# Kernel tuning notes

Hardware: AMD Instinct MI355X
Metric: run time of the kernel (lower is better)

The kernel has to match this reference:

```python
import jax, jax.numpy as jnp
import numpy as np
from jax import lax

EMBED_DIM = 384
NUM_GROUPS = 128
GROUP_SIZE = 64
LN_EPS = 1e-5


def setup_inputs() -> dict:
    key = jax.random.key(0)
    k_pts, k1, k2, k3, k4 = jax.random.split(key, 5)
    B, N = 32, 16384
    points = jax.random.normal(k_pts, (B, N, 3), dtype=jnp.float32)
    # local_mlp: Linear(3,128) -> GELU -> Linear(128, embed_dim)
    w1 = jax.random.normal(k1, (3, 128), dtype=jnp.float32) * (1.0 / np.sqrt(3))
    b1 = jax.random.normal(k2, (128,), dtype=jnp.float32) * 0.01
    w2 = jax.random.normal(k3, (128, EMBED_DIM), dtype=jnp.float32) * (1.0 / np.sqrt(128))
    b2 = jax.random.normal(k4, (EMBED_DIM,), dtype=jnp.float32) * 0.01
    ln_scale = jnp.ones((EMBED_DIM,), dtype=jnp.float32)
    ln_bias = jnp.zeros((EMBED_DIM,), dtype=jnp.float32)
    return {"points": points, "w1": w1, "b1": b1, "w2": w2, "b2": b2,
            "ln_scale": ln_scale, "ln_bias": ln_bias}


def _farthest_point_sample(points, num_samples):
    # points: [B, N, 3]. Deterministic start at index 0 (torch uses randint).
    B, N, _ = points.shape

    def step(carry, _):
        distance, farthest = carry  # [B, N], [B]
        centroid = jnp.take_along_axis(points, farthest[:, None, None], axis=1)  # [B,1,3]
        d = jnp.sum((points - centroid) ** 2, axis=-1)  # [B, N]
        distance = jnp.minimum(distance, d)
        nxt = jnp.argmax(distance, axis=-1).astype(jnp.int32)
        return (distance, nxt), farthest

    init = (jnp.full((B, N), jnp.inf, dtype=points.dtype),
            jnp.zeros((B,), dtype=jnp.int32))
    _, idx = lax.scan(step, init, None, length=num_samples)  # [S, B]
    return idx.T  # [B, S]


def reference(points, w1, b1, w2, b2, ln_scale, ln_bias):
    B, N, _ = points.shape
    centroid_idx = _farthest_point_sample(points, NUM_GROUPS)  # [B, G]
    centroids = jnp.take_along_axis(
        points, centroid_idx[:, :, None].astype(jnp.int32), axis=1)  # [B, G, 3]

    # squared distances (same ordering as torch.cdist for topk); matmul form
    # avoids materializing a [B, G, N, 3] diff tensor.
    c2 = jnp.sum(centroids ** 2, axis=-1)  # [B, G]
    p2 = jnp.sum(points ** 2, axis=-1)     # [B, N]
    dist2 = c2[:, :, None] + p2[:, None, :] - 2.0 * jnp.einsum(
        'bgc,bnc->bgn', centroids, points)  # [B, G, N]

    # k smallest -> top_k of negated distances
    _, neighbor_idx = lax.top_k(-dist2, GROUP_SIZE)  # [B, G, K]

    batch_ix = jnp.arange(B)[:, None, None]
    grouped = points[batch_ix, neighbor_idx]  # [B, G, K, 3]
    local_coords = grouped - centroids[:, :, None, :]  # [B, G, K, 3]

    h = jax.nn.gelu(local_coords @ w1 + b1, approximate=False)  # [B,G,K,128]
    feats = h @ w2 + b2  # [B, G, K, D]
    tokens = jnp.mean(feats, axis=2)  # [B, G, D]

    mu = jnp.mean(tokens, axis=-1, keepdims=True)
    var = jnp.mean((tokens - mu) ** 2, axis=-1, keepdims=True)
    tokens_ln = (tokens - mu) * lax.rsqrt(var + LN_EPS) * ln_scale + ln_bias
    return centroids, tokens_ln
```

## Files before the change

### kernel.cpp

```cpp
#include <hip/hip_runtime.h>
#include <math.h>

#define BB 32
#define NN 16384
#define GG 128
#define KK 64
#define HH 128
#define DD 384
#define LN_EPS 1e-5f
#define NBUCK 2048
#define CANDCAP 1024

__device__ __forceinline__ float sq3(float x, float y, float z) {
    return __fadd_rn(__fadd_rn(__fmul_rn(x, x), __fmul_rn(y, y)), __fmul_rn(z, z));
}

__device__ __forceinline__ unsigned distkey(float px, float py, float pz, float4 c4) {
    float p2 = sq3(px, py, pz);
    float dot = __fadd_rn(__fadd_rn(__fmul_rn(c4.x, px), __fmul_rn(c4.y, py)),
                          __fmul_rn(c4.z, pz));
    float d = __fsub_rn(__fadd_rn(c4.w, p2), __fmul_rn(2.0f, dot));
    unsigned u = __float_as_uint(d);
    return u ^ ((u & 0x80000000u) ? 0xFFFFFFFFu : 0x80000000u);
}

__global__ void prep_kernel(const float* __restrict__ w2, float* __restrict__ w2t) {
    int i = blockIdx.x * 256 + threadIdx.x;
    if (i < HH * DD) {
        int f = i >> 7;
        int k = i & 127;
        w2t[i] = w2[k * DD + f];
    }
}

__global__ __launch_bounds__(512, 2) void fps_kernel(const float* __restrict__ pts,
                                                     float* __restrict__ cent_out,
                                                     float4* __restrict__ cent_pad) {
    const int b = blockIdx.x;
    const int tid = threadIdx.x;
    const float* p = pts + (size_t)b * NN * 3;
    const float4* p4 = (const float4*)p;

    float x[32], y[32], z[32], dist[32];
#pragma unroll
    for (int j = 0; j < 8; j++) {
        int q = j * 512 + tid;
        float4 A = p4[3 * q], B = p4[3 * q + 1], C = p4[3 * q + 2];
        x[j * 4 + 0] = A.x; y[j * 4 + 0] = A.y; z[j * 4 + 0] = A.z;
        x[j * 4 + 1] = A.w; y[j * 4 + 1] = B.x; z[j * 4 + 1] = B.y;
        x[j * 4 + 2] = B.z; y[j * 4 + 2] = B.w; z[j * 4 + 2] = C.x;
        x[j * 4 + 3] = C.y; y[j * 4 + 3] = C.z; z[j * 4 + 3] = C.w;
#pragma unroll
        for (int t = 0; t < 4; t++) dist[j * 4 + t] = INFINITY;
    }

    __shared__ unsigned long long slot[GG];
    for (int i = tid; i < GG; i += 512) slot[i] = 0ull;
    __syncthreads();

    float cx = p[0], cy = p[1], cz = p[2];

    for (int it = 0; it < GG; it++) {
        if (tid == 0) {
            float* co = cent_out + ((size_t)b * GG + it) * 3;
            co[0] = cx; co[1] = cy; co[2] = cz;
            cent_pad[b * GG + it] = make_float4(cx, cy, cz, sq3(cx, cy, cz));
        }
        if (it == GG - 1) break;

        float bv0 = -INFINITY, bv1 = -INFINITY, bv2 = -INFINITY, bv3 = -INFINITY;
        int bi0 = 0, bi1 = 0, bi2 = 0, bi3 = 0;
#pragma unroll
        for (int j = 0; j < 8; j++) {
            int nb = 4 * (j * 512 + tid);
#pragma unroll
            for (int t = 0; t < 4; t++) {
                int r = j * 4 + t;
                float dx = __fsub_rn(x[r], cx);
                float dy = __fsub_rn(y[r], cy);
                float dz = __fsub_rn(z[r], cz);
                float d = sq3(dx, dy, dz);
                float dj = fminf(dist[r], d);
                dist[r] = dj;
                int n = nb + t;
                switch (t) {
                    case 0: if (dj > bv0) { bv0 = dj; bi0 = n; } break;
                    case 1: if (dj > bv1) { bv1 = dj; bi1 = n; } break;
                    case 2: if (dj > bv2) { bv2 = dj; bi2 = n; } break;
                    case 3: if (dj > bv3) { bv3 = dj; bi3 = n; } break;
                }
            }
        }
        float fv = bv0; int fi = bi0;
        if (bv1 > fv || (bv1 == fv && bi1 < fi)) { fv = bv1; fi = bi1; }
        if (bv2 > fv || (bv2 == fv && bi2 < fi)) { fv = bv2; fi = bi2; }
        if (bv3 > fv || (bv3 == fv && bi3 < fi)) { fv = bv3; fi = bi3; }
#pragma unroll
        for (int off = 32; off >= 1; off >>= 1) {
            float ov = __shfl_down(fv, off);
            int oi = __shfl_down(fi, off);
            if (ov > fv || (ov == fv && oi < fi)) { fv = ov; fi = oi; }
        }
        if ((tid & 63) == 0) {
            unsigned long long packed =
                ((unsigned long long)__float_as_uint(fv) << 32) |
                (unsigned)(0xFFFFFFFFu - (unsigned)fi);
            atomicMax(&slot[it], packed);
        }
        __syncthreads();
        unsigned long long w = slot[it];
        int idx = (int)(0xFFFFFFFFu - (unsigned)w);
        const float* wp = p + (size_t)idx * 3;
        cx = wp[0]; cy = wp[1]; cz = wp[2];
    }
}

__global__ __launch_bounds__(256, 6) void group_kernel(
    const float* __restrict__ pts, const float4* __restrict__ cent_pad,
    const float* __restrict__ w1, const float* __restrict__ b1,
    const float* __restrict__ w2t, const float* __restrict__ b2,
    const float* __restrict__ lns, const float* __restrict__ lnb,
    float* __restrict__ tok_out) {
    __shared__ __align__(16) union {
        unsigned hist[NBUCK];
        unsigned long long cand[CANDCAP];
    } sh;
    __shared__ int selIdx[KK];
    __shared__ float4 localPt[KK];
    __shared__ float w1s[3 * HH];
    __shared__ float b1s[HH];
    __shared__ __align__(16) float hbar[HH];
    __shared__ float partial[256];
    __shared__ float red2[8];
    __shared__ float toks[DD];
    __shared__ int waveSum[4];
    __shared__ unsigned long long wmin[4];
    __shared__ unsigned TA_S;
    __shared__ int cntS;
    __shared__ unsigned long long lastS;
    __shared__ float muS, rstdS;

    const int tid = threadIdx.x;
    int bid = blockIdx.x;
    int xcd = bid & 7, sub = bid >> 3;
    int b = xcd * 4 + (sub >> 7);
    int g = sub & 127;

    const float* p = pts + (size_t)b * NN * 3;
    const float4* p4 = (const float4*)p;
    float4 c4 = cent_pad[b * GG + g];

    for (int i = tid; i < 3 * HH; i += 256) w1s[i] = w1[i];
    if (tid < HH) b1s[tid] = b1[tid];
    for (int i = tid; i < NBUCK; i += 256) sh.hist[i] = 0;
    if (tid == 0) cntS = 0;
    __syncthreads();

    for (int i = 0; i < 16; i++) {
        int t4 = i * 256 + tid;
        float4 A = p4[3 * t4], B = p4[3 * t4 + 1], C = p4[3 * t4 + 2];
        unsigned k0 = distkey(A.x, A.y, A.z, c4);
        unsigned k1 = distkey(A.w, B.x, B.y, c4);
        unsigned k2 = distkey(B.z, B.w, C.x, c4);
        unsigned k3 = distkey(C.y, C.z, C.w, c4);
        atomicAdd(&sh.hist[k0 >> 21], 1u);
        atomicAdd(&sh.hist[k1 >> 21], 1u);
        atomicAdd(&sh.hist[k2 >> 21], 1u);
        atomicAdd(&sh.hist[k3 >> 21], 1u);
    }
    __syncthreads();

    {
        uint4 h0 = ((const uint4*)sh.hist)[tid * 2];
        uint4 h1 = ((const uint4*)sh.hist)[tid * 2 + 1];
        int loc[8] = {(int)h0.x, (int)h0.y, (int)h0.z, (int)h0.w,
                      (int)h1.x, (int)h1.y, (int)h1.z, (int)h1.w};
        int s = 0;
#pragma unroll
        for (int j = 0; j < 8; j++) s += loc[j];
        int lane = tid & 63, wid = tid >> 6;
        int v = s;
#pragma unroll
        for (int off = 1; off < 64; off <<= 1) {
            int o = __shfl_up(v, off);
            if (lane >= off) v += o;
        }
        if (lane == 63) waveSum[wid] = v;
        __syncthreads();
        int base = 0;
        for (int w = 0; w < wid; w++) base += waveSum[w];
        int c = base + v - s;
#pragma unroll
        for (int j = 0; j < 8; j++) {
            if (c < KK && c + loc[j] >= KK) TA_S = (unsigned)(tid * 8 + j);
            c += loc[j];
        }
        __syncthreads();
    }
    unsigned TA = TA_S;

    for (int i = 0; i < 16; i++) {
        int t4 = i * 256 + tid;
        float4 A = p4[3 * t4], B = p4[3 * t4 + 1], C = p4[3 * t4 + 2];
        unsigned k[4];
        k[0] = distkey(A.x, A.y, A.z, c4);
        k[1] = distkey(A.w, B.x, B.y, c4);
        k[2] = distkey(B.z, B.w, C.x, c4);
        k[3] = distkey(C.y, C.z, C.w, c4);
#pragma unroll
        for (int q = 0; q < 4; q++) {
            if ((k[q] >> 21) <= TA) {
                int pos = atomicAdd(&cntS, 1);
                if (pos < CANDCAP)
                    sh.cand[pos] =
                        ((unsigned long long)k[q] << 32) | (unsigned)(4 * t4 + q);
            }
        }
    }
    __syncthreads();
    int cnt = cntS;

    if (cnt <= CANDCAP) {
        for (int c0 = tid; c0 < cnt; c0 += 256) {
            unsigned long long pr = sh.cand[c0];
            int rank = 0;
            for (int j = 0; j < cnt; j++) rank += (sh.cand[j] < pr);
            if (rank < KK) selIdx[rank] = (int)(unsigned)pr;
        }
        __syncthreads();
    } else {
        if (tid == 0) lastS = 0ull;
        __syncthreads();
        for (int r = 0; r < KK; r++) {
            unsigned long long last = lastS;
            unsigned long long best = 0xFFFFFFFFFFFFFFFFull;
            for (int i = 0; i < 16; i++) {
                int t4 = i * 256 + tid;
                float4 A = p4[3 * t4], B = p4[3 * t4 + 1], C = p4[3 * t4 + 2];
                unsigned k[4];
                k[0] = distkey(A.x, A.y, A.z, c4);
                k[1] = distkey(A.w, B.x, B.y, c4);
                k[2] = distkey(B.z, B.w, C.x, c4);
                k[3] = distkey(C.y, C.z, C.w, c4);
#pragma unroll
                for (int q = 0; q < 4; q++) {
                    unsigned long long pr =
                        ((unsigned long long)k[q] << 32) | (unsigned)(4 * t4 + q);
                    if ((r == 0 || pr > last) && pr < best) best = pr;
                }
            }
            unsigned blo = (unsigned)best, bhi = (unsigned)(best >> 32);
#pragma unroll
            for (int off = 32; off >= 1; off >>= 1) {
                unsigned olo = __shfl_down(blo, off);
                unsigned ohi = __shfl_down(bhi, off);
                unsigned long long ob = ((unsigned long long)ohi << 32) | olo;
                unsigned long long cur = ((unsigned long long)bhi << 32) | blo;
                if (ob < cur) { blo = olo; bhi = ohi; }
            }
            int lane = tid & 63, wid = tid >> 6;
            if (lane == 0) wmin[wid] = ((unsigned long long)bhi << 32) | blo;
            __syncthreads();
            if (tid == 0) {
                unsigned long long m = wmin[0];
                for (int w = 1; w < 4; w++) if (wmin[w] < m) m = wmin[w];
                selIdx[r] = (int)(unsigned)m;
                lastS = m;
            }
            __syncthreads();
        }
    }

    if (tid < KK) {
        int n = selIdx[tid];
        float px = p[n * 3], py = p[n * 3 + 1], pz = p[n * 3 + 2];
        localPt[tid] = make_float4(px - c4.x, py - c4.y, pz - c4.z, 0.f);
    }
    __syncthreads();
    {
        int f = tid & 127, half = tid >> 7;
        float wa = w1s[f], wb = w1s[HH + f], wc = w1s[2 * HH + f], bb = b1s[f];
        float s = 0.f;
        for (int k = half * 32; k < half * 32 + 32; k++) {
            float4 lp = localPt[k];
            float a = lp.x * wa + lp.y * wb + lp.z * wc + bb;
            float hh = 0.5f * a * (1.0f + erff(a * 0.70710678118654752440f));
            s += hh;
        }
        partial[tid] = s;
    }
    __syncthreads();
    if (tid < HH) hbar[tid] = (partial[tid] + partial[tid + HH]) * (1.0f / 64.0f);
    __syncthreads();
    for (int f2 = tid; f2 < DD; f2 += 256) {
        const float4* wrow = (const float4*)(w2t + f2 * HH);
        const float4* hb = (const float4*)hbar;
        float acc = b2[f2];
#pragma unroll 8
        for (int q = 0; q < 32; q++) {
            float4 w4 = wrow[q];
            float4 h4 = hb[q];
            acc += h4.x * w4.x + h4.y * w4.y + h4.z * w4.z + h4.w * w4.w;
        }
        toks[f2] = acc;
    }
    __syncthreads();
    {
        float s1 = 0.f, s2 = 0.f;
        for (int f2 = tid; f2 < DD; f2 += 256) {
            float v = toks[f2];
            s1 += v;
            s2 += v * v;
        }
#pragma unroll
        for (int off = 32; off >= 1; off >>= 1) {
            s1 += __shfl_down(s1, off);
            s2 += __shfl_down(s2, off);
        }
        int lane = tid & 63, wid = tid >> 6;
        if (lane == 0) { partial[wid] = s1; red2[wid] = s2; }
        __syncthreads();
        if (tid == 0) {
            float t1 = partial[0] + partial[1] + partial[2] + partial[3];
            float t2 = red2[0] + red2[1] + red2[2] + red2[3];
            float mu = t1 / (float)DD;
            float var = t2 / (float)DD - mu * mu;
            muS = mu;
            rstdS = rsqrtf(var + LN_EPS);
        }
        __syncthreads();
    }
    float mu = muS, rstd = rstdS;
    float* outp = tok_out + ((size_t)b * GG + g) * DD;
    for (int f2 = tid; f2 < DD; f2 += 256) {
        outp[f2] = (toks[f2] - mu) * rstd * lns[f2] + lnb[f2];
    }
}

extern "C" void kernel_launch(void* const* d_in, const int* in_sizes, int n_in,
                              void* d_out, int out_size, void* d_ws, size_t ws_size,
                              hipStream_t stream) {
    const float* pts = (const float*)d_in[0];
    const float* w1 = (const float*)d_in[1];
    const float* b1 = (const float*)d_in[2];
    const float* w2 = (const float*)d_in[3];
    const float* b2 = (const float*)d_in[4];
    const float* lns = (const float*)d_in[5];
    const float* lnb = (const float*)d_in[6];
    float* out = (float*)d_out;

    float4* cent_pad = (float4*)d_ws;
    float* w2t = (float*)((char*)d_ws + BB * GG * sizeof(float4));

    prep_kernel<<<192, 256, 0, stream>>>(w2, w2t);
    fps_kernel<<<BB, 512, 0, stream>>>(pts, out, cent_pad);
    group_kernel<<<BB * GG, 256, 0, stream>>>(pts, cent_pad, w1, b1, w2t, b2, lns, lnb,
                                              out + BB * GG * 3);
}
```

Measured before the change: 531.7 us.

## Split farthest-point sampling across eight blocks per batch with global-memory barrier

Farthest-point sampling now runs on 8 cooperating blocks per batch of 256 threads each, instead of one 512-thread block, so 256 blocks occupy many more CUs. Each block finds its local farthest point, writes a packed key and the point's coordinates to global memory, and spins on an atomic counter until all 8 slices arrive. All blocks then reduce the 8 candidates redundantly. Carrying the coordinates through the reduction removes the dependent global load of the winner's coordinates. The cost is a per-iteration inter-block spin barrier through L2, which relies on all 256 blocks being co-resident to avoid deadlock.

```diff
diff --git a/kernel.cpp b/kernel.cpp
--- a/kernel.cpp
+++ b/kernel.cpp
@@ -10,6 +10,7 @@
 #define LN_EPS 1e-5f
 #define NBUCK 2048
 #define CANDCAP 1024
+#define SPB 8
 
 __device__ __forceinline__ float sq3(float x, float y, float z) {
     return __fadd_rn(__fadd_rn(__fmul_rn(x, x), __fmul_rn(y, y)), __fmul_rn(z, z));
@@ -24,27 +25,32 @@
     return u ^ ((u & 0x80000000u) ? 0xFFFFFFFFu : 0x80000000u);
 }
 
-__global__ void prep_kernel(const float* __restrict__ w2, float* __restrict__ w2t) {
+__global__ void prep_kernel(const float* __restrict__ w2, float* __restrict__ w2t,
+                            unsigned* __restrict__ cnt) {
     int i = blockIdx.x * 256 + threadIdx.x;
     if (i < HH * DD) {
         int f = i >> 7;
         int k = i & 127;
         w2t[i] = w2[k * DD + f];
     }
-}
-
-__global__ __launch_bounds__(512, 2) void fps_kernel(const float* __restrict__ pts,
-                                                     float* __restrict__ cent_out,
-                                                     float4* __restrict__ cent_pad) {
-    const int b = blockIdx.x;
+    if (i < BB * GG) cnt[i] = 0;
+}
+
+__global__ __launch_bounds__(256) void fps_kernel(
+    const float* __restrict__ pts, float* __restrict__ cent_out,
+    float4* __restrict__ cent_pad, unsigned long long* __restrict__ candK,
+    float4* __restrict__ candP, unsigned* __restrict__ cnt) {
+    const int blk = blockIdx.x;
+    const int b = blk >> 3;
+    const int s = blk & 7;
     const int tid = threadIdx.x;
     const float* p = pts + (size_t)b * NN * 3;
     const float4* p4 = (const float4*)p;
 
-    float x[32], y[32], z[32], dist[32];
-#pragma unroll
-    for (int j = 0; j < 8; j++) {
-        int q = j * 512 + tid;
+    float x[8], y[8], z[8], dist[8];
+#pragma unroll
+    for (int j = 0; j < 2; j++) {
+        int q = s * 512 + j * 256 + tid;
         float4 A = p4[3 * q], B = p4[3 * q + 1], C = p4[3 * q + 2];
         x[j * 4 + 0] = A.x; y[j * 4 + 0] = A.y; z[j * 4 + 0] = A.z;
         x[j * 4 + 1] = A.w; y[j * 4 + 1] = B.x; z[j * 4 + 1] = B.y;
@@ -54,25 +60,24 @@
         for (int t = 0; t < 4; t++) dist[j * 4 + t] = INFINITY;
     }
 
-    __shared__ unsigned long long slot[GG];
-    for (int i = tid; i < GG; i += 512) slot[i] = 0ull;
-    __syncthreads();
+    __shared__ unsigned long long wkey[4];
+    __shared__ float4 wc[4];
 
     float cx = p[0], cy = p[1], cz = p[2];
 
     for (int it = 0; it < GG; it++) {
-        if (tid == 0) {
+        if (s == 0 && tid == 0) {
             float* co = cent_out + ((size_t)b * GG + it) * 3;
             co[0] = cx; co[1] = cy; co[2] = cz;
             cent_pad[b * GG + it] = make_float4(cx, cy, cz, sq3(cx, cy, cz));
         }
         if (it == GG - 1) break;
 
-        float bv0 = -INFINITY, bv1 = -INFINITY, bv2 = -INFINITY, bv3 = -INFINITY;
-        int bi0 = 0, bi1 = 0, bi2 = 0, bi3 = 0;
-#pragma unroll
-        for (int j = 0; j < 8; j++) {
-            int nb = 4 * (j * 512 + tid);
+        float fv = -INFINITY, fx = 0.f, fy = 0.f, fz = 0.f;
+        int fi = 0;
+#pragma unroll
+        for (int j = 0; j < 2; j++) {
+            int nb = 4 * (s * 512 + j * 256 + tid);
 #pragma unroll
             for (int t = 0; t < 4; t++) {
                 int r = j * 4 + t;
@@ -82,36 +87,58 @@
                 float d = sq3(dx, dy, dz);
                 float dj = fminf(dist[r], d);
                 dist[r] = dj;
-                int n = nb + t;
-                switch (t) {
-                    case 0: if (dj > bv0) { bv0 = dj; bi0 = n; } break;
-                    case 1: if (dj > bv1) { bv1 = dj; bi1 = n; } break;
-                    case 2: if (dj > bv2) { bv2 = dj; bi2 = n; } break;
-                    case 3: if (dj > bv3) { bv3 = dj; bi3 = n; } break;
-                }
-            }
-        }
-        float fv = bv0; int fi = bi0;
-        if (bv1 > fv || (bv1 == fv && bi1 < fi)) { fv = bv1; fi = bi1; }
-        if (bv2 > fv || (bv2 == fv && bi2 < fi)) { fv = bv2; fi = bi2; }
-        if (bv3 > fv || (bv3 == fv && bi3 < fi)) { fv = bv3; fi = bi3; }
+                if (dj > fv) { fv = dj; fi = nb + t; fx = x[r]; fy = y[r]; fz = z[r]; }
+            }
+        }
 #pragma unroll
         for (int off = 32; off >= 1; off >>= 1) {
             float ov = __shfl_down(fv, off);
             int oi = __shfl_down(fi, off);
-            if (ov > fv || (ov == fv && oi < fi)) { fv = ov; fi = oi; }
-        }
-        if ((tid & 63) == 0) {
-            unsigned long long packed =
-                ((unsigned long long)__float_as_uint(fv) << 32) |
-                (unsigned)(0xFFFFFFFFu - (unsigned)fi);
-            atomicMax(&slot[it], packed);
-        }
-        __syncthreads();
-        unsigned long long w = slot[it];
-        int idx = (int)(0xFFFFFFFFu - (unsigned)w);
-        const float* wp = p + (size_t)idx * 3;
-        cx = wp[0]; cy = wp[1]; cz = wp[2];
+            float ox = __shfl_down(fx, off);
+            float oy = __shfl_down(fy, off);
+            float oz = __shfl_down(fz, off);
+            if (ov > fv || (ov == fv && oi < fi)) {
+                fv = ov; fi = oi; fx = ox; fy = oy; fz = oz;
+            }
+        }
+        int lane = tid & 63, wid = tid >> 6;
+        if (lane == 0) {
+            wkey[wid] = ((unsigned long long)__float_as_uint(fv) << 32) |
+                        (unsigned)(0xFFFFFFFFu - (unsigned)fi);
+            wc[wid] = make_float4(fx, fy, fz, 0.f);
+        }
+        __syncthreads();
+
+        const int slot = b * GG + it;
+        if (tid == 0) {
+            unsigned long long bk = wkey[0];
+            float4 bc = wc[0];
+#pragma unroll
+            for (int w = 1; w < 4; w++) {
+                unsigned long long k2 = wkey[w];
+                if (k2 > bk) { bk = k2; bc = wc[w]; }
+            }
+            candK[slot * SPB + s] = bk;
+            candP[slot * SPB + s] = bc;
+            __hip_atomic_fetch_add(&cnt[slot], 1u, __ATOMIC_RELEASE,
+                                   __HIP_MEMORY_SCOPE_AGENT);
+            while (__hip_atomic_load(&cnt[slot], __ATOMIC_ACQUIRE,
+                                     __HIP_MEMORY_SCOPE_AGENT) < SPB)
+                __builtin_amdgcn_s_sleep(1);
+        }
+        __syncthreads();
+
+        {
+            unsigned long long bk = candK[slot * SPB];
+            float4 bc = candP[slot * SPB];
+#pragma unroll
+            for (int w = 1; w < SPB; w++) {
+                unsigned long long k2 = candK[slot * SPB + w];
+                float4 c2 = candP[slot * SPB + w];
+                if (k2 > bk) { bk = k2; bc = c2; }
+            }
+            cx = bc.x; cy = bc.y; cz = bc.z;
+        }
     }
 }
 
@@ -350,10 +377,13 @@
     float* out = (float*)d_out;
 
     float4* cent_pad = (float4*)d_ws;
-    float* w2t = (float*)((char*)d_ws + BB * GG * sizeof(float4));
-
-    prep_kernel<<<192, 256, 0, stream>>>(w2, w2t);
-    fps_kernel<<<BB, 512, 0, stream>>>(pts, out, cent_pad);
+    float* w2t = (float*)((char*)d_ws + 64 * 1024);
+    unsigned long long* candK = (unsigned long long*)((char*)d_ws + 256 * 1024);
+    float4* candP = (float4*)((char*)d_ws + 512 * 1024);
+    unsigned* cnt = (unsigned*)((char*)d_ws + 1024 * 1024);
+
+    prep_kernel<<<192, 256, 0, stream>>>(w2, w2t, cnt);
+    fps_kernel<<<BB * SPB, 256, 0, stream>>>(pts, out, cent_pad, candK, candP, cnt);
     group_kernel<<<BB * GG, 256, 0, stream>>>(pts, cent_pad, w1, b1, w2t, b2, lns, lnb,
                                               out + BB * GG * 3);
 }
```

Measured after the change: 1.134 ms. +113.3%, slower.

## Fuse FPS and grouping into one kernel with progress-flag producer/consumer overlap

Applied to the files above, without the earlier changes.

Merges the farthest-point-sampling and grouping kernels into one launch. The first 32 blocks run FPS at raised priority and publish each centroid plus a per-batch progress counter with agent-scope atomics. The remaining blocks spin-wait on that counter, so kNN grouping for early centroids overlaps the serial FPS iterations instead of waiting for all of FPS to finish. Grouping blocks are widened to 512 threads, with two independent centroid-groups per block using split shared memory. The fused path relies on the FPS blocks being resident (deadlock risk if they are not scheduled) and adds spin-wait and memory-ordering overhead.

```diff
diff --git a/kernel.cpp b/kernel.cpp
--- a/kernel.cpp
+++ b/kernel.cpp
@@ -24,183 +24,237 @@
     return u ^ ((u & 0x80000000u) ? 0xFFFFFFFFu : 0x80000000u);
 }
 
-__global__ void prep_kernel(const float* __restrict__ w2, float* __restrict__ w2t) {
+__global__ void prep_kernel(const float* __restrict__ w2, float* __restrict__ w2t,
+                            unsigned* __restrict__ prog) {
     int i = blockIdx.x * 256 + threadIdx.x;
     if (i < HH * DD) {
         int f = i >> 7;
         int k = i & 127;
         w2t[i] = w2[k * DD + f];
     }
+    if (i < BB) prog[i] = 0;
 }
 
-__global__ __launch_bounds__(512, 2) void fps_kernel(const float* __restrict__ pts,
-                                                     float* __restrict__ cent_out,
-                                                     float4* __restrict__ cent_pad) {
-    const int b = blockIdx.x;
+struct GrpSh {
+    union {
+        unsigned hist[2][NBUCK];
+        unsigned long long cand[2][CANDCAP];
+    } u;
+    int selIdx[2][KK];
+    float4 localPt[2][KK];
+    float w1s[3 * HH];
+    float b1s[HH];
+    float hbar[2][HH];
+    float partial[2][256];
+    float red2[2][4];
+    float toks[2][DD];
+    int waveSum[2][4];
+    unsigned long long wmin[2][4];
+    unsigned TA_S[2];
+    int cntS[2];
+    unsigned long long lastS[2];
+    float muS[2], rstdS[2];
+    float4 c4s[2];
+    int fbS;
+};
+struct FpsSh {
+    unsigned long long slot[GG];
+};
+
+__global__ __launch_bounds__(512, 6) void fused_kernel(
+    const float* __restrict__ pts, const float* __restrict__ w1,
+    const float* __restrict__ b1, const float* __restrict__ w2t,
+    const float* __restrict__ b2, const float* __restrict__ lns,
+    const float* __restrict__ lnb, float* __restrict__ cent_out,
+    float4* __restrict__ cent_pad, float* __restrict__ tok_out,
+    unsigned* __restrict__ prog) {
+    __shared__ union {
+        FpsSh f;
+        GrpSh g;
+    } sh;
     const int tid = threadIdx.x;
+
+    if (blockIdx.x < BB) {
+        __builtin_amdgcn_s_setprio(3);
+        const int b = blockIdx.x;
+        const float* p = pts + (size_t)b * NN * 3;
+        const float4* p4 = (const float4*)p;
+
+        float x[32], y[32], z[32], dist[32];
+#pragma unroll
+        for (int j = 0; j < 8; j++) {
+            int q = j * 512 + tid;
+            float4 A = p4[3 * q], B = p4[3 * q + 1], C = p4[3 * q + 2];
+            x[j * 4 + 0] = A.x; y[j * 4 + 0] = A.y; z[j * 4 + 0] = A.z;
+            x[j * 4 + 1] = A.w; y[j * 4 + 1] = B.x; z[j * 4 + 1] = B.y;
+            x[j * 4 + 2] = B.z; y[j * 4 + 2] = B.w; z[j * 4 + 2] = C.x;
+            x[j * 4 + 3] = C.y; y[j * 4 + 3] = C.z; z[j * 4 + 3] = C.w;
+#pragma unroll
+            for (int t = 0; t < 4; t++) dist[j * 4 + t] = INFINITY;
+        }
+
+        for (int i = tid; i < GG; i += 512) sh.f.slot[i] = 0ull;
+        __syncthreads();
+
+        float cx = p[0], cy = p[1], cz = p[2];
+
+        for (int it = 0; it < GG; it++) {
+            if (tid == 0) {
+                if (it > 0) {
+                    asm volatile("s_waitcnt vmcnt(0)" ::: "memory");
+                    __hip_atomic_store(&prog[b], (unsigned)it, __ATOMIC_RELAXED,
+                                       __HIP_MEMORY_SCOPE_AGENT);
+                }
+                float* co = cent_out + ((size_t)b * GG + it) * 3;
+                co[0] = cx; co[1] = cy; co[2] = cz;
+                float c2v = sq3(cx, cy, cz);
+                unsigned long long lo =
+                    ((unsigned long long)__float_as_uint(cy) << 32) | __float_as_uint(cx);
+                unsigned long long hi =
+                    ((unsigned long long)__float_as_uint(c2v) << 32) | __float_as_uint(cz);
+                unsigned long long* cp =
+                    (unsigned long long*)&cent_pad[(size_t)b * GG + it];
+                __hip_atomic_store(cp, lo, __ATOMIC_RELAXED, __HIP_MEMORY_SCOPE_AGENT);
+                __hip_atomic_store(cp + 1, hi, __ATOMIC_RELAXED, __HIP_MEMORY_SCOPE_AGENT);
+            }
+            if (it == GG - 1) break;
+
+            float bv0 = -INFINITY, bv1 = -INFINITY, bv2 = -INFINITY, bv3 = -INFINITY;
+            int bi0 = 0, bi1 = 0, bi2 = 0, bi3 = 0;
+#pragma unroll
+            for (int j = 0; j < 8; j++) {
+                int nb = 4 * (j * 512 + tid);
+#pragma unroll
+                for (int t = 0; t < 4; t++) {
+                    int r = j * 4 + t;
+                    float dx = __fsub_rn(x[r], cx);
+                    float dy = __fsub_rn(y[r], cy);
+                    float dz = __fsub_rn(z[r], cz);
+                    float d = sq3(dx, dy, dz);
+                    float dj = fminf(dist[r], d);
+                    dist[r] = dj;
+                    int n = nb + t;
+                    switch (t) {
+                        case 0: if (dj > bv0) { bv0 = dj; bi0 = n; } break;
+                        case 1: if (dj > bv1) { bv1 = dj; bi1 = n; } break;
+                        case 2: if (dj > bv2) { bv2 = dj; bi2 = n; } break;
+                        case 3: if (dj > bv3) { bv3 = dj; bi3 = n; } break;
+                    }
+                }
+            }
+            float fv = bv0; int fi = bi0;
+            if (bv1 > fv || (bv1 == fv && bi1 < fi)) { fv = bv1; fi = bi1; }
+            if (bv2 > fv || (bv2 == fv && bi2 < fi)) { fv = bv2; fi = bi2; }
+            if (bv3 > fv || (bv3 == fv && bi3 < fi)) { fv = bv3; fi = bi3; }
+#pragma unroll
+            for (int off = 32; off >= 1; off >>= 1) {
+                float ov = __shfl_down(fv, off);
+                int oi = __shfl_down(fi, off);
+                if (ov > fv || (ov == fv && oi < fi)) { fv = ov; fi = oi; }
+            }
+            if ((tid & 63) == 0) {
+                unsigned long long packed =
+                    ((unsigned long long)__float_as_uint(fv) << 32) |
+                    (unsigned)(0xFFFFFFFFu - (unsigned)fi);
+                atomicMax(&sh.f.slot[it], packed);
+            }
+            __syncthreads();
+            unsigned long long w = sh.f.slot[it];
+            int idx = (int)(0xFFFFFFFFu - (unsigned)w);
+            const float* wp = p + (size_t)idx * 3;
+            cx = wp[0]; cy = wp[1]; cz = wp[2];
+        }
+        if (tid == 0) {
+            asm volatile("s_waitcnt vmcnt(0)" ::: "memory");
+            __hip_atomic_store(&prog[b], (unsigned)GG, __ATOMIC_RELAXED,
+                               __HIP_MEMORY_SCOPE_AGENT);
+        }
+        return;
+    }
+
+    const int h = tid & 255;
+    const int half = tid >> 8;
+    const int lane = h & 63, wid = h >> 6;
+
+    int bid = blockIdx.x - BB;
+    int x = bid & 7;
+    int r = bid >> 3;
+    int g = r >> 1;
+    int pairSel = r & 1;
+    int b = x * 4 + pairSel * 2 + half;
+
     const float* p = pts + (size_t)b * NN * 3;
     const float4* p4 = (const float4*)p;
 
-    float x[32], y[32], z[32], dist[32];
-#pragma unroll
-    for (int j = 0; j < 8; j++) {
-        int q = j * 512 + tid;
-        float4 A = p4[3 * q], B = p4[3 * q + 1], C = p4[3 * q + 2];
-        x[j * 4 + 0] = A.x; y[j * 4 + 0] = A.y; z[j * 4 + 0] = A.z;
-        x[j * 4 + 1] = A.w; y[j * 4 + 1] = B.x; z[j * 4 + 1] = B.y;
-        x[j * 4 + 2] = B.z; y[j * 4 + 2] = B.w; z[j * 4 + 2] = C.x;
-        x[j * 4 + 3] = C.y; y[j * 4 + 3] = C.z; z[j * 4 + 3] = C.w;
-#pragma unroll
-        for (int t = 0; t < 4; t++) dist[j * 4 + t] = INFINITY;
-    }
-
-    __shared__ unsigned long long slot[GG];
-    for (int i = tid; i < GG; i += 512) slot[i] = 0ull;
-    __syncthreads();
-
-    float cx = p[0], cy = p[1], cz = p[2];
-
-    for (int it = 0; it < GG; it++) {
-        if (tid == 0) {
-            float* co = cent_out + ((size_t)b * GG + it) * 3;
-            co[0] = cx; co[1] = cy; co[2] = cz;
-            cent_pad[b * GG + it] = make_float4(cx, cy, cz, sq3(cx, cy, cz));
-        }
-        if (it == GG - 1) break;
-
-        float bv0 = -INFINITY, bv1 = -INFINITY, bv2 = -INFINITY, bv3 = -INFINITY;
-        int bi0 = 0, bi1 = 0, bi2 = 0, bi3 = 0;
-#pragma unroll
-        for (int j = 0; j < 8; j++) {
-            int nb = 4 * (j * 512 + tid);
-#pragma unroll
-            for (int t = 0; t < 4; t++) {
-                int r = j * 4 + t;
-                float dx = __fsub_rn(x[r], cx);
-                float dy = __fsub_rn(y[r], cy);
-                float dz = __fsub_rn(z[r], cz);
-                float d = sq3(dx, dy, dz);
-                float dj = fminf(dist[r], d);
-                dist[r] = dj;
-                int n = nb + t;
-                switch (t) {
-                    case 0: if (dj > bv0) { bv0 = dj; bi0 = n; } break;
-                    case 1: if (dj > bv1) { bv1 = dj; bi1 = n; } break;
-                    case 2: if (dj > bv2) { bv2 = dj; bi2 = n; } break;
-                    case 3: if (dj > bv3) { bv3 = dj; bi3 = n; } break;
-                }
-            }
-        }
-        float fv = bv0; int fi = bi0;
-        if (bv1 > fv || (bv1 == fv && bi1 < fi)) { fv = bv1; fi = bi1; }
-        if (bv2 > fv || (bv2 == fv && bi2 < fi)) { fv = bv2; fi = bi2; }
-        if (bv3 > fv || (bv3 == fv && bi3 < fi)) { fv = bv3; fi = bi3; }
-#pragma unroll
-        for (int off = 32; off >= 1; off >>= 1) {
-            float ov = __shfl_down(fv, off);
-            int oi = __shfl_down(fi, off);
-            if (ov > fv || (ov == fv && oi < fi)) { fv = ov; fi = oi; }
-        }
-        if ((tid & 63) == 0) {
-            unsigned long long packed =
-                ((unsigned long long)__float_as_uint(fv) << 32) |
-                (unsigned)(0xFFFFFFFFu - (unsigned)fi);
-            atomicMax(&slot[it], packed);
-        }
-        __syncthreads();
-        unsigned long long w = slot[it];
-        int idx = (int)(0xFFFFFFFFu - (unsigned)w);
-        const float* wp = p + (size_t)idx * 3;
-        cx = wp[0]; cy = wp[1]; cz = wp[2];
-    }
-}
-
-__global__ __launch_bounds__(256, 6) void group_kernel(
-    const float* __restrict__ pts, const float4* __restrict__ cent_pad,
-    const float* __restrict__ w1, const float* __restrict__ b1,
-    const float* __restrict__ w2t, const float* __restrict__ b2,
-    const float* __restrict__ lns, const float* __restrict__ lnb,
-    float* __restrict__ tok_out) {
-    __shared__ __align__(16) union {
-        unsigned hist[NBUCK];
-        unsigned long long cand[CANDCAP];
-    } sh;
-    __shared__ int selIdx[KK];
-    __shared__ float4 localPt[KK];
-    __shared__ float w1s[3 * HH];
-    __shared__ float b1s[HH];
-    __shared__ __align__(16) float hbar[HH];
-    __shared__ float partial[256];
-    __shared__ float red2[8];
-    __shared__ float toks[DD];
-    __shared__ int waveSum[4];
-    __shared__ unsigned long long wmin[4];
-    __shared__ unsigned TA_S;
-    __shared__ int cntS;
-    __shared__ unsigned long long lastS;
-    __shared__ float muS, rstdS;
-
-    const int tid = threadIdx.x;
-    int bid = blockIdx.x;
-    int xcd = bid & 7, sub = bid >> 3;
-    int b = xcd * 4 + (sub >> 7);
-    int g = sub & 127;
-
-    const float* p = pts + (size_t)b * NN * 3;
-    const float4* p4 = (const float4*)p;
-    float4 c4 = cent_pad[b * GG + g];
-
-    for (int i = tid; i < 3 * HH; i += 256) w1s[i] = w1[i];
-    if (tid < HH) b1s[tid] = b1[tid];
-    for (int i = tid; i < NBUCK; i += 256) sh.hist[i] = 0;
-    if (tid == 0) cntS = 0;
-    __syncthreads();
+    for (int i = tid; i < 3 * HH; i += 512) sh.g.w1s[i] = w1[i];
+    if (tid < HH) sh.g.b1s[tid] = b1[tid];
+    for (int i = h; i < NBUCK; i += 256) sh.g.u.hist[half][i] = 0;
+    if (h == 0) sh.g.cntS[half] = 0;
+    if (tid == 0) sh.g.fbS = 0;
+
+    if (h == 0) {
+        unsigned need = (unsigned)(g + 1);
+        while (__hip_atomic_load(&prog[b], __ATOMIC_RELAXED,
+                                 __HIP_MEMORY_SCOPE_AGENT) < need)
+            __builtin_amdgcn_s_sleep(32);
+        asm volatile("" ::: "memory");
+        const unsigned long long* cp =
+            (const unsigned long long*)&cent_pad[(size_t)b * GG + g];
+        unsigned long long lo =
+            __hip_atomic_load(cp, __ATOMIC_RELAXED, __HIP_MEMORY_SCOPE_AGENT);
+        unsigned long long hi =
+            __hip_atomic_load(cp + 1, __ATOMIC_RELAXED, __HIP_MEMORY_SCOPE_AGENT);
+        sh.g.c4s[half] = make_float4(
+            __uint_as_float((unsigned)lo), __uint_as_float((unsigned)(lo >> 32)),
+            __uint_as_float((unsigned)hi), __uint_as_float((unsigned)(hi >> 32)));
+    }
+    __syncthreads();
+    float4 c4 = sh.g.c4s[half];
 
     for (int i = 0; i < 16; i++) {
-        int t4 = i * 256 + tid;
+        int t4 = i * 256 + h;
         float4 A = p4[3 * t4], B = p4[3 * t4 + 1], C = p4[3 * t4 + 2];
         unsigned k0 = distkey(A.x, A.y, A.z, c4);
         unsigned k1 = distkey(A.w, B.x, B.y, c4);
         unsigned k2 = distkey(B.z, B.w, C.x, c4);
         unsigned k3 = distkey(C.y, C.z, C.w, c4);
-        atomicAdd(&sh.hist[k0 >> 21], 1u);
-        atomicAdd(&sh.hist[k1 >> 21], 1u);
-        atomicAdd(&sh.hist[k2 >> 21], 1u);
-        atomicAdd(&sh.hist[k3 >> 21], 1u);
+        atomicAdd(&sh.g.u.hist[half][k0 >> 21], 1u);
+        atomicAdd(&sh.g.u.hist[half][k1 >> 21], 1u);
+        atomicAdd(&sh.g.u.hist[half][k2 >> 21], 1u);
+        atomicAdd(&sh.g.u.hist[half][k3 >> 21], 1u);
     }
     __syncthreads();
 
     {
-        uint4 h0 = ((const uint4*)sh.hist)[tid * 2];
-        uint4 h1 = ((const uint4*)sh.hist)[tid * 2 + 1];
+        uint4 h0 = ((const uint4*)sh.g.u.hist[half])[h * 2];
+        uint4 h1 = ((const uint4*)sh.g.u.hist[half])[h * 2 + 1];
         int loc[8] = {(int)h0.x, (int)h0.y, (int)h0.z, (int)h0.w,
                       (int)h1.x, (int)h1.y, (int)h1.z, (int)h1.w};
         int s = 0;
 #pragma unroll
         for (int j = 0; j < 8; j++) s += loc[j];
-        int lane = tid & 63, wid = tid >> 6;
         int v = s;
 #pragma unroll
         for (int off = 1; off < 64; off <<= 1) {
             int o = __shfl_up(v, off);
             if (lane >= off) v += o;
         }
-        if (lane == 63) waveSum[wid] = v;
+        if (lane == 63) sh.g.waveSum[half][wid] = v;
         __syncthreads();
         int base = 0;
-        for (int w = 0; w < wid; w++) base += waveSum[w];
+        for (int w = 0; w < wid; w++) base += sh.g.waveSum[half][w];
         int c = base + v - s;
 #pragma unroll
         for (int j = 0; j < 8; j++) {
-            if (c < KK && c + loc[j] >= KK) TA_S = (unsigned)(tid * 8 + j);
+            if (c < KK && c + loc[j] >= KK) sh.g.TA_S[half] = (unsigned)(h * 8 + j);
             c += loc[j];
         }
         __syncthreads();
     }
-    unsigned TA = TA_S;
+    unsigned TA = sh.g.TA_S[half];
 
     for (int i = 0; i < 16; i++) {
-        int t4 = i * 256 + tid;
+        int t4 = i * 256 + h;
         float4 A = p4[3 * t4], B = p4[3 * t4 + 1], C = p4[3 * t4 + 2];
         unsigned k[4];
         k[0] = distkey(A.x, A.y, A.z, c4);
@@ -210,32 +264,35 @@
 #pragma unroll
         for (int q = 0; q < 4; q++) {
             if ((k[q] >> 21) <= TA) {
-                int pos = atomicAdd(&cntS, 1);
+                int pos = atomicAdd(&sh.g.cntS[half], 1);
                 if (pos < CANDCAP)
-                    sh.cand[pos] =
+                    sh.g.u.cand[half][pos] =
                         ((unsigned long long)k[q] << 32) | (unsigned)(4 * t4 + q);
             }
         }
     }
     __syncthreads();
-    int cnt = cntS;
-
-    if (cnt <= CANDCAP) {
-        for (int c0 = tid; c0 < cnt; c0 += 256) {
-            unsigned long long pr = sh.cand[c0];
+    int cnt = sh.g.cntS[half];
+    if (h == 0 && cnt > CANDCAP) sh.g.fbS = 1;
+    __syncthreads();
+    int fb = sh.g.fbS;
+
+    if (!fb) {
+        for (int c0 = h; c0 < cnt; c0 += 256) {
+            unsigned long long pr = sh.g.u.cand[half][c0];
             int rank = 0;
-            for (int j = 0; j < cnt; j++) rank += (sh.cand[j] < pr);
-            if (rank < KK) selIdx[rank] = (int)(unsigned)pr;
+            for (int j = 0; j < cnt; j++) rank += (sh.g.u.cand[half][j] < pr);
+            if (rank < KK) sh.g.selIdx[half][rank] = (int)(unsigned)pr;
         }
         __syncthreads();
     } else {
-        if (tid == 0) lastS = 0ull;
-        __syncthreads();
-        for (int r = 0; r < KK; r++) {
-            unsigned long long last = lastS;
+        if (h == 0) sh.g.lastS[half] = 0ull;
+        __syncthreads();
+        for (int rr = 0; rr < KK; rr++) {
+            unsigned long long last = sh.g.lastS[half];
             unsigned long long best = 0xFFFFFFFFFFFFFFFFull;
             for (int i = 0; i < 16; i++) {
-                int t4 = i * 256 + tid;
+                int t4 = i * 256 + h;
                 float4 A = p4[3 * t4], B = p4[3 * t4 + 1], C = p4[3 * t4 + 2];
                 unsigned k[4];
                 k[0] = distkey(A.x, A.y, A.z, c4);
@@ -246,7 +303,7 @@
                 for (int q = 0; q < 4; q++) {
                     unsigned long long pr =
                         ((unsigned long long)k[q] << 32) | (unsigned)(4 * t4 + q);
-                    if ((r == 0 || pr > last) && pr < best) best = pr;
+                    if ((rr == 0 || pr > last) && pr < best) best = pr;
                 }
             }
             unsigned blo = (unsigned)best, bhi = (unsigned)(best >> 32);
@@ -258,43 +315,46 @@
                 unsigned long long cur = ((unsigned long long)bhi << 32) | blo;
                 if (ob < cur) { blo = olo; bhi = ohi; }
             }
-            int lane = tid & 63, wid = tid >> 6;
-            if (lane == 0) wmin[wid] = ((unsigned long long)bhi << 32) | blo;
+            if (lane == 0) sh.g.wmin[half][wid] = ((unsigned long long)bhi << 32) | blo;
             __syncthreads();
-            if (tid == 0) {
-                unsigned long long m = wmin[0];
-                for (int w = 1; w < 4; w++) if (wmin[w] < m) m = wmin[w];
-                selIdx[r] = (int)(unsigned)m;
-                lastS = m;
+            if (h == 0) {
+                unsigned long long m = sh.g.wmin[half][0];
+                for (int w = 1; w < 4; w++)
+                    if (sh.g.wmin[half][w] < m) m = sh.g.wmin[half][w];
+                sh.g.selIdx[half][rr] = (int)(unsigned)m;
+                sh.g.lastS[half] = m;
             }
             __syncthreads();
         }
     }
 
-    if (tid < KK) {
-        int n = selIdx[tid];
+    if (h < KK) {
+        int n = sh.g.selIdx[half][h];
         float px = p[n * 3], py = p[n * 3 + 1], pz = p[n * 3 + 2];
-        localPt[tid] = make_float4(px - c4.x, py - c4.y, pz - c4.z, 0.f);
+        sh.g.localPt[half][h] = make_float4(px - c4.x, py - c4.y, pz - c4.z, 0.f);
     }
     __syncthreads();
     {
-        int f = tid & 127, half = tid >> 7;
-        float wa = w1s[f], wb = w1s[HH + f], wc = w1s[2 * HH + f], bb = b1s[f];
+        int f = h & 127, halfk = h >> 7;
+        float wa = sh.g.w1s[f], wb = sh.g.w1s[HH + f], wc = sh.g.w1s[2 * HH + f];
+        float bb = sh.g.b1s[f];
         float s = 0.f;
-        for (int k = half * 32; k < half * 32 + 32; k++) {
-            float4 lp = localPt[k];
+        for (int k = halfk * 32; k < halfk * 32 + 32; k++) {
+            float4 lp = sh.g.localPt[half][k];
             float a = lp.x * wa + lp.y * wb + lp.z * wc + bb;
             float hh = 0.5f * a * (1.0f + erff(a * 0.70710678118654752440f));
             s += hh;
         }
-        partial[tid] = s;
-    }
-    __syncthreads();
-    if (tid < HH) hbar[tid] = (partial[tid] + partial[tid + HH]) * (1.0f / 64.0f);
-    __syncthreads();
-    for (int f2 = tid; f2 < DD; f2 += 256) {
+        sh.g.partial[half][h] = s;
+    }
+    __syncthreads();
+    if (h < HH)
+        sh.g.hbar[half][h] =
+            (sh.g.partial[half][h] + sh.g.partial[half][h + HH]) * (1.0f / 64.0f);
+    __syncthreads();
+    for (int f2 = h; f2 < DD; f2 += 256) {
         const float4* wrow = (const float4*)(w2t + f2 * HH);
-        const float4* hb = (const float4*)hbar;
+        const float4* hb = (const float4*)sh.g.hbar[half];
         float acc = b2[f2];
 #pragma unroll 8
         for (int q = 0; q < 32; q++) {
@@ -302,13 +362,13 @@
             float4 h4 = hb[q];
             acc += h4.x * w4.x + h4.y * w4.y + h4.z * w4.z + h4.w * w4.w;
         }
-        toks[f2] = acc;
+        sh.g.toks[half][f2] = acc;
     }
     __syncthreads();
     {
         float s1 = 0.f, s2 = 0.f;
-        for (int f2 = tid; f2 < DD; f2 += 256) {
-            float v = toks[f2];
+        for (int f2 = h; f2 < DD; f2 += 256) {
+            float v = sh.g.toks[half][f2];
             s1 += v;
             s2 += v * v;
         }
@@ -317,23 +377,24 @@
             s1 += __shfl_down(s1, off);
             s2 += __shfl_down(s2, off);
         }
-        int lane = tid & 63, wid = tid >> 6;
-        if (lane == 0) { partial[wid] = s1; red2[wid] = s2; }
-        __syncthreads();
-        if (tid == 0) {
-            float t1 = partial[0] + partial[1] + partial[2] + partial[3];
-            float t2 = red2[0] + red2[1] + red2[2] + red2[3];
+        if (lane == 0) { sh.g.partial[half][wid] = s1; sh.g.red2[half][wid] = s2; }
+        __syncthreads();
+        if (h == 0) {
+            float t1 = sh.g.partial[half][0] + sh.g.partial[half][1] +
+                       sh.g.partial[half][2] + sh.g.partial[half][3];
+            float t2 = sh.g.red2[half][0] + sh.g.red2[half][1] + sh.g.red2[half][2] +
+                       sh.g.red2[half][3];
             float mu = t1 / (float)DD;
             float var = t2 / (float)DD - mu * mu;
-            muS = mu;
-            rstdS = rsqrtf(var + LN_EPS);
-        }
-        __syncthreads();
-    }
-    float mu = muS, rstd = rstdS;
+            sh.g.muS[half] = mu;
+            sh.g.rstdS[half] = rsqrtf(var + LN_EPS);
+        }
+        __syncthreads();
+    }
+    float mu = sh.g.muS[half], rstd = sh.g.rstdS[half];
     float* outp = tok_out + ((size_t)b * GG + g) * DD;
-    for (int f2 = tid; f2 < DD; f2 += 256) {
-        outp[f2] = (toks[f2] - mu) * rstd * lns[f2] + lnb[f2];
+    for (int f2 = h; f2 < DD; f2 += 256) {
+        outp[f2] = (sh.g.toks[half][f2] - mu) * rstd * lns[f2] + lnb[f2];
     }
 }
 
@@ -350,10 +411,10 @@
     float* out = (float*)d_out;
 
     float4* cent_pad = (float4*)d_ws;
-    float* w2t = (float*)((char*)d_ws + BB * GG * sizeof(float4));
-
-    prep_kernel<<<192, 256, 0, stream>>>(w2, w2t);
-    fps_kernel<<<BB, 512, 0, stream>>>(pts, out, cent_pad);
-    group_kernel<<<BB * GG, 256, 0, stream>>>(pts, cent_pad, w1, b1, w2t, b2, lns, lnb,
-                                              out + BB * GG * 3);
+    float* w2t = (float*)((char*)d_ws + 64 * 1024);
+    unsigned* prog = (unsigned*)((char*)d_ws + 256 * 1024);
+
+    prep_kernel<<<192, 256, 0, stream>>>(w2, w2t, prog);
+    fused_kernel<<<BB + (BB * GG) / 2, 512, 0, stream>>>(
+        pts, w1, b1, w2t, b2, lns, lnb, out, cent_pad, out + BB * GG * 3, prog);
 }
```

Measured after the change: 1.717 ms. 223% more time.

## Double FPS block size and replace atomic slot with per-wave winner broadcast

Applied to the files above, without the earlier changes.

The farthest-point-sampling kernel now runs 1024 threads per batch with 16 points per thread instead of 512 threads with 32. Each iteration ends with the winning lane of every wave writing its packed key and the winner's coordinates from registers into shared memory. All threads then scan the 16 wave keys, which replaces the shared atomicMax and the dependent global load of the new centroid. This shortens the serial per-iteration latency and raises parallelism for this 32-block kernel, at the cost of a second barrier per iteration and a linear scan over the wave results.

```diff
diff --git a/kernel.cpp b/kernel.cpp
--- a/kernel.cpp
+++ b/kernel.cpp
@@ -33,18 +33,18 @@
     }
 }
 
-__global__ __launch_bounds__(512, 2) void fps_kernel(const float* __restrict__ pts,
-                                                     float* __restrict__ cent_out,
-                                                     float4* __restrict__ cent_pad) {
+__global__ __launch_bounds__(1024, 4) void fps_kernel(const float* __restrict__ pts,
+                                                      float* __restrict__ cent_out,
+                                                      float4* __restrict__ cent_pad) {
     const int b = blockIdx.x;
     const int tid = threadIdx.x;
     const float* p = pts + (size_t)b * NN * 3;
     const float4* p4 = (const float4*)p;
 
-    float x[32], y[32], z[32], dist[32];
-#pragma unroll
-    for (int j = 0; j < 8; j++) {
-        int q = j * 512 + tid;
+    float x[16], y[16], z[16], dist[16];
+#pragma unroll
+    for (int j = 0; j < 4; j++) {
+        int q = j * 1024 + tid;
         float4 A = p4[3 * q], B = p4[3 * q + 1], C = p4[3 * q + 2];
         x[j * 4 + 0] = A.x; y[j * 4 + 0] = A.y; z[j * 4 + 0] = A.z;
         x[j * 4 + 1] = A.w; y[j * 4 + 1] = B.x; z[j * 4 + 1] = B.y;
@@ -54,11 +54,11 @@
         for (int t = 0; t < 4; t++) dist[j * 4 + t] = INFINITY;
     }
 
-    __shared__ unsigned long long slot[GG];
-    for (int i = tid; i < GG; i += 512) slot[i] = 0ull;
-    __syncthreads();
+    __shared__ unsigned long long wkey[16];
+    __shared__ float wx[16], wy[16], wz[16];
 
     float cx = p[0], cy = p[1], cz = p[2];
+    const int wid = tid >> 6;
 
     for (int it = 0; it < GG; it++) {
         if (tid == 0) {
@@ -71,8 +71,8 @@
         float bv0 = -INFINITY, bv1 = -INFINITY, bv2 = -INFINITY, bv3 = -INFINITY;
         int bi0 = 0, bi1 = 0, bi2 = 0, bi3 = 0;
 #pragma unroll
-        for (int j = 0; j < 8; j++) {
-            int nb = 4 * (j * 512 + tid);
+        for (int j = 0; j < 4; j++) {
+            int nb = 4 * (j * 1024 + tid);
 #pragma unroll
             for (int t = 0; t < 4; t++) {
                 int r = j * 4 + t;
@@ -91,27 +91,46 @@
                 }
             }
         }
-        float fv = bv0; int fi = bi0;
-        if (bv1 > fv || (bv1 == fv && bi1 < fi)) { fv = bv1; fi = bi1; }
-        if (bv2 > fv || (bv2 == fv && bi2 < fi)) { fv = bv2; fi = bi2; }
-        if (bv3 > fv || (bv3 == fv && bi3 < fi)) { fv = bv3; fi = bi3; }
+        float mfv = bv0; int mfi = bi0;
+        if (bv1 > mfv || (bv1 == mfv && bi1 < mfi)) { mfv = bv1; mfi = bi1; }
+        if (bv2 > mfv || (bv2 == mfv && bi2 < mfi)) { mfv = bv2; mfi = bi2; }
+        if (bv3 > mfv || (bv3 == mfv && bi3 < mfi)) { mfv = bv3; mfi = bi3; }
+
+        float fv = mfv; int fi = mfi;
 #pragma unroll
         for (int off = 32; off >= 1; off >>= 1) {
             float ov = __shfl_down(fv, off);
             int oi = __shfl_down(fi, off);
             if (ov > fv || (ov == fv && oi < fi)) { fv = ov; fi = oi; }
         }
-        if ((tid & 63) == 0) {
-            unsigned long long packed =
-                ((unsigned long long)__float_as_uint(fv) << 32) |
-                (unsigned)(0xFFFFFFFFu - (unsigned)fi);
-            atomicMax(&slot[it], packed);
-        }
-        __syncthreads();
-        unsigned long long w = slot[it];
-        int idx = (int)(0xFFFFFFFFu - (unsigned)w);
-        const float* wp = p + (size_t)idx * 3;
-        cx = wp[0]; cy = wp[1]; cz = wp[2];
+        int wfi = __shfl(fi, 0);
+        if (mfi == wfi) {
+            int jj = (wfi >> 2) - tid;
+            int tt = wfi & 3;
+            float sx = 0.f, sy = 0.f, sz = 0.f;
+#pragma unroll
+            for (int j = 0; j < 4; j++) {
+                if (jj == j * 1024) {
+#pragma unroll
+                    for (int t = 0; t < 4; t++) {
+                        if (tt == t) { sx = x[j * 4 + t]; sy = y[j * 4 + t]; sz = z[j * 4 + t]; }
+                    }
+                }
+            }
+            wkey[wid] = ((unsigned long long)__float_as_uint(mfv) << 32) |
+                        (unsigned)(0xFFFFFFFFu - (unsigned)mfi);
+            wx[wid] = sx; wy[wid] = sy; wz[wid] = sz;
+        }
+        __syncthreads();
+        unsigned long long bk = wkey[0];
+        int bw = 0;
+#pragma unroll
+        for (int w = 1; w < 16; w++) {
+            unsigned long long k2 = wkey[w];
+            if (k2 > bk) { bk = k2; bw = w; }
+        }
+        cx = wx[bw]; cy = wy[bw]; cz = wz[bw];
+        __syncthreads();
     }
 }
 
@@ -353,7 +372,7 @@
     float* w2t = (float*)((char*)d_ws + BB * GG * sizeof(float4));
 
     prep_kernel<<<192, 256, 0, stream>>>(w2, w2t);
-    fps_kernel<<<BB, 512, 0, stream>>>(pts, out, cent_pad);
+    fps_kernel<<<BB, 1024, 0, stream>>>(pts, out, cent_pad);
     group_kernel<<<BB * GG, 256, 0, stream>>>(pts, cent_pad, w1, b1, w2t, b2, lns, lnb,
                                               out + BB * GG * 3);
 }
```

New measurement: 665.0 us. 1.25x slower.
